# Kernel tuning notes

Hardware: AMD Instinct MI355X
Metric: run time of the kernel (lower is better)

The kernel has to match this reference:

```python
import jax, jax.numpy as jnp
import numpy as np

N = 100000
E = 1600000
H = 128
L = 3


def setup_inputs() -> dict:
    key = jax.random.key(0)
    ks = jax.random.split(key, 8)
    z = jax.random.normal(ks[0], (N, H), dtype=jnp.float32)
    edge_index = jax.random.randint(ks[1], (2, E), 0, N, dtype=jnp.int64)
    edge_weight = jax.random.uniform(ks[2], (E,), dtype=jnp.float32)
    s = 1.0 / np.sqrt(H)
    weight = jax.random.uniform(ks[3], (L, H, H), minval=-s, maxval=s, dtype=jnp.float32)
    w_ih = jax.random.uniform(ks[4], (3 * H, H), minval=-s, maxval=s, dtype=jnp.float32)
    w_hh = jax.random.uniform(ks[5], (3 * H, H), minval=-s, maxval=s, dtype=jnp.float32)
    b_ih = jax.random.uniform(ks[6], (3 * H,), minval=-s, maxval=s, dtype=jnp.float32)
    b_hh = jax.random.uniform(ks[7], (3 * H,), minval=-s, maxval=s, dtype=jnp.float32)
    return {"z": z, "edge_weight": edge_weight, "weight": weight,
            "w_ih": w_ih, "w_hh": w_hh, "b_ih": b_ih, "b_hh": b_hh,
            "edge_index": edge_index}


def _gru_cell(m, h, w_ih, w_hh, b_ih, b_hh):
    # torch GRUCell: gate order (r, z, n)
    gi = m @ w_ih.T + b_ih   # [N, 3H]
    gh = h @ w_hh.T + b_hh   # [N, 3H]
    i_r, i_z, i_n = jnp.split(gi, 3, axis=-1)
    h_r, h_z, h_n = jnp.split(gh, 3, axis=-1)
    r = jax.nn.sigmoid(i_r + h_r)
    zg = jax.nn.sigmoid(i_z + h_z)
    n = jnp.tanh(i_n + r * h_n)
    return (1.0 - zg) * n + zg * h


def reference(z, edge_weight, weight, w_ih, w_hh, b_ih, b_hh, edge_index):
    src = edge_index[0]  # x_j gathered from source nodes
    dst = edge_index[1]  # aggregated at target nodes
    x = z  # in_channels == out_channels, so no zero padding needed
    for l in range(L):
        m = x @ weight[l]                                  # [N, H]
        msg = m[src] * edge_weight[:, None]                # [E, H]
        agg = jax.ops.segment_sum(msg, dst, num_segments=N)  # aggr='add'
        x = _gru_cell(agg, x, w_ih, w_hh, b_ih, b_hh)
    return x
```

## Files before the change

kernel.cpp:

```cpp
#include <hip/hip_runtime.h>

typedef __bf16 bf16x8 __attribute__((ext_vector_type(8)));
typedef float floatx4 __attribute__((ext_vector_type(4)));

#define NPB 256
#define NPB_SHIFT 8
#define MAXNB 1024
#define TILE 4096

static __device__ __forceinline__ float bfu_to_f(unsigned short u) {
    unsigned int x = ((unsigned int)u) << 16;
    return __builtin_bit_cast(float, x);
}
static __device__ __forceinline__ unsigned short f_to_bfu(float f) {
    unsigned int u = __builtin_bit_cast(unsigned int, f);
    unsigned int r = (u + 0x7fffu + ((u >> 16) & 1u)) >> 16;
    return (unsigned short)r;
}

__global__ void detect_k(const unsigned short* __restrict__ bih_u,
                         const unsigned int* __restrict__ ei_u,
                         int* __restrict__ flags) {
    if (threadIdx.x == 0 && blockIdx.x == 0) {
        int votes = 0;
        for (int i = 0; i < 64; i++) {
            unsigned short u = bih_u[2 * i];
            unsigned int ex = (u >> 7) & 0xFF;
            if (ex >= 64 && ex < 124) votes++;
        }
        flags[0] = (votes >= 48) ? 1 : 0;
        int zeros = 0;
        for (int i = 0; i < 64; i++) {
            if (ei_u[2 * i + 1] == 0u) zeros++;
        }
        flags[1] = (zeros == 64) ? 1 : 0;
    }
}


__global__ void cvt_bf16_k(const void* __restrict__ in, unsigned short* __restrict__ out,
                           int n, const int* __restrict__ flags) {
    int i = blockIdx.x * 256 + threadIdx.x;
    if (i >= n) return;
    if (flags[0]) out[i] = ((const unsigned short*)in)[i];
    else out[i] = f_to_bfu(((const float*)in)[i]);
}

__global__ void cvt_bias_k(const void* __restrict__ bih, const void* __restrict__ bhh,
                           float* __restrict__ bih_f, float* __restrict__ bhh_f,
                           const int* __restrict__ flags) {
    int i = blockIdx.x * 256 + threadIdx.x;
    if (i >= 768) return;
    const void* src = (i < 384) ? bih : bhh;
    int j = (i < 384) ? i : i - 384;
    float v = flags[0] ? bfu_to_f(((const unsigned short*)src)[j]) : ((const float*)src)[j];
    if (i < 384) bih_f[j] = v;
    else bhh_f[j] = v;
}

__global__ void out_k(const unsigned short* __restrict__ xb, void* __restrict__ out,
                      int n, const int* __restrict__ flags) {
    int i = blockIdx.x * 256 + threadIdx.x;
    if (i >= n) return;
    if (flags[0]) ((unsigned short*)out)[i] = xb[i];
    else ((float*)out)[i] = bfu_to_f(xb[i]);
}


static __device__ __forceinline__ int load_idx(const unsigned int* eiu, size_t pos, int is64) {
    return (int)eiu[is64 ? 2 * pos : pos];
}

__global__ __launch_bounds__(256) void count_k(const unsigned int* __restrict__ eiu,
                                               int* __restrict__ bucketCnt, int E,
                                               const int* __restrict__ flags) {
    __shared__ int cnt[MAXNB];
    int t = threadIdx.x;
    for (int b = t; b < MAXNB; b += 256) cnt[b] = 0;
    __syncthreads();
    int is64 = flags[1];
    int e0 = blockIdx.x * TILE;
    int e1 = min(e0 + TILE, E);
    for (int e = e0 + t; e < e1; e += 256) {
        int d = load_idx(eiu, (size_t)E + e, is64);
        atomicAdd(&cnt[d >> NPB_SHIFT], 1);
    }
    __syncthreads();
    for (int b = t; b < MAXNB; b += 256) {
        int c = cnt[b];
        if (c) atomicAdd(&bucketCnt[b], c);
    }
}

__global__ void scanB_k(const int* __restrict__ bucketCnt, int* __restrict__ bucketBase,
                        int* __restrict__ bucketCursor, int NB, int E) {
    __shared__ int sh[MAXNB];
    int t = threadIdx.x;
    int v = (t < NB) ? bucketCnt[t] : 0;
    sh[t] = v;
    __syncthreads();
    for (int off = 1; off < MAXNB; off <<= 1) {
        int u = (t >= off) ? sh[t - off] : 0;
        __syncthreads();
        sh[t] += u;
        __syncthreads();
    }
    if (t < NB) {
        int b = sh[t] - v;
        bucketBase[t] = b;
        bucketCursor[t] = b;
    }
    if (t == 0) bucketBase[NB] = E;
}

__global__ __launch_bounds__(256) void bin_k(const unsigned int* __restrict__ eiu,
                                             const void* __restrict__ ew,
                                             int* __restrict__ bucketCursor,
                                             uint2* __restrict__ rec8,
                                             int* __restrict__ dstA, int E,
                                             const int* __restrict__ flags) {
    __shared__ int cnt[MAXNB];
    __shared__ int basel[MAXNB];
    int t = threadIdx.x;
    for (int b = t; b < MAXNB; b += 256) cnt[b] = 0;
    __syncthreads();
    int is64 = flags[1];
    int isb = flags[0];
    int e0 = blockIdx.x * TILE;
    int e1 = min(e0 + TILE, E);
    for (int e = e0 + t; e < e1; e += 256) {
        int d = load_idx(eiu, (size_t)E + e, is64);
        atomicAdd(&cnt[d >> NPB_SHIFT], 1);
    }
    __syncthreads();
    for (int b = t; b < MAXNB; b += 256) {
        int c = cnt[b];
        basel[b] = c ? atomicAdd(&bucketCursor[b], c) : 0;
        cnt[b] = 0;
    }
    __syncthreads();
    for (int e = e0 + t; e < e1; e += 256) {
        int s = load_idx(eiu, (size_t)e, is64);
        int d = load_idx(eiu, (size_t)E + e, is64);
        float w = isb ? bfu_to_f(((const unsigned short*)ew)[e]) : ((const float*)ew)[e];
        int b = d >> NPB_SHIFT;
        int p = basel[b] + atomicAdd(&cnt[b], 1);
        dstA[p] = d;
        rec8[p] = make_uint2((unsigned int)s, __builtin_bit_cast(unsigned int, w));
    }
}

__global__ __launch_bounds__(256) void csr_k(const uint2* __restrict__ rec8,
                                             const int* __restrict__ dstA,
                                             const int* __restrict__ bucketBase,
                                             int* __restrict__ offsets,
                                             uint2* __restrict__ rec, int N, int E) {
    __shared__ int cnt[NPB];
    __shared__ int sh[NPB];
    __shared__ int cur[NPB];
    int t = threadIdx.x;
    int b = blockIdx.x;
    int n0 = b << NPB_SHIFT;
    int nodes = min(NPB, N - n0);
    int ebase = bucketBase[b];
    int ecnt = bucketBase[b + 1] - ebase;

    cnt[t] = 0;
    __syncthreads();
    for (int i = t; i < ecnt; i += 256) {
        int d = dstA[ebase + i] - n0;
        atomicAdd(&cnt[d], 1);
    }
    __syncthreads();
    int v = cnt[t];
    sh[t] = v;
    __syncthreads();
    for (int off = 1; off < NPB; off <<= 1) {
        int u = (t >= off) ? sh[t - off] : 0;
        __syncthreads();
        sh[t] += u;
        __syncthreads();
    }
    int loff = sh[t] - v;
    if (t < nodes) offsets[n0 + t] = ebase + loff;
    cur[t] = ebase + loff;
    if (b == 0 && t == 0) offsets[N] = E;
    __syncthreads();
    for (int i = t; i < ecnt; i += 256) {
        int d = dstA[ebase + i] - n0;
        int p = atomicAdd(&cur[d], 1);
        rec[p] = rec8[ebase + i];
    }
}


static __device__ __forceinline__ float dot8_bf(uint4 wv, uint4 iv) {
    float s;
    s  = bfu_to_f((unsigned short)(wv.x)) * bfu_to_f((unsigned short)(iv.x));
    s += bfu_to_f((unsigned short)(wv.x >> 16)) * bfu_to_f((unsigned short)(iv.x >> 16));
    s += bfu_to_f((unsigned short)(wv.y)) * bfu_to_f((unsigned short)(iv.y));
    s += bfu_to_f((unsigned short)(wv.y >> 16)) * bfu_to_f((unsigned short)(iv.y >> 16));
    s += bfu_to_f((unsigned short)(wv.z)) * bfu_to_f((unsigned short)(iv.z));
    s += bfu_to_f((unsigned short)(wv.z >> 16)) * bfu_to_f((unsigned short)(iv.z >> 16));
    s += bfu_to_f((unsigned short)(wv.w)) * bfu_to_f((unsigned short)(iv.w));
    s += bfu_to_f((unsigned short)(wv.w >> 16)) * bfu_to_f((unsigned short)(iv.w >> 16));
    return s;
}

__global__ void make_ut_k(const void* __restrict__ weight, const void* __restrict__ wih,
                          unsigned short* __restrict__ Ut, const int* __restrict__ flags) {
    int idx = blockIdx.x * 256 + threadIdx.x;
    if (idx >= 3 * 384 * 128) return;
    int isb = flags[0];
    int a = idx & 127;
    int j = (idx >> 7) % 384;
    int l = idx / (384 * 128);
    float s = 0.f;
    if (isb) {
        const uint4* W4 = (const uint4*)((const unsigned short*)weight + (size_t)l * 16384 + a * 128);
        const uint4* I4 = (const uint4*)((const unsigned short*)wih + (size_t)j * 128);
#pragma unroll
        for (int c = 0; c < 16; c++) s += dot8_bf(W4[c], I4[c]);
    } else {
        const float4* W4 = (const float4*)((const float*)weight + (size_t)l * 16384 + a * 128);
        const float4* I4 = (const float4*)((const float*)wih + (size_t)j * 128);
#pragma unroll
        for (int c = 0; c < 32; c++) {
            float4 w = W4[c], i = I4[c];
            s += w.x * i.x + w.y * i.y + w.z * i.z + w.w * i.w;
        }
    }
    Ut[idx] = f_to_bfu(s);
}

__global__ void pack_b_k(const unsigned short* __restrict__ Ut,
                         const void* __restrict__ whh,
                         unsigned short* __restrict__ Bp,
                         const int* __restrict__ flags) {
    int idx = blockIdx.x * 256 + threadIdx.x;
    if (idx >= 3 * 48 * 4 * 64) return;
    int l = idx / 12288;
    int rem = idx % 12288;
    int ct = rem >> 8;
    int kc = (rem >> 6) & 3;
    int lane = rem & 63;
    int col = (ct % 24) * 16 + (lane & 15);
    int k = kc * 32 + (lane >> 4) * 8;
    unsigned short tmp[8];
    const unsigned short* src;
    if (ct < 24) {
        src = Ut + (size_t)l * 49152 + col * 128 + k;
    } else if (flags[0]) {
        src = (const unsigned short*)whh + (size_t)col * 128 + k;
    } else {
        const float* wf = (const float*)whh + (size_t)col * 128 + k;
        for (int i = 0; i < 8; i++) tmp[i] = f_to_bfu(wf[i]);
        src = tmp;
    }
    unsigned short* dst = Bp + (size_t)l * 98304 + ((size_t)(ct * 4 + kc) * 64 + lane) * 8;
    for (int i = 0; i < 8; i++) dst[i] = src[i];
}


__global__ __launch_bounds__(256) void agg_k(const unsigned short* __restrict__ xb,
                                             const int* __restrict__ offs,
                                             const uint2* __restrict__ rec,
                                             unsigned short* __restrict__ y, int N) {
    int node = (int)((blockIdx.x * 256 + threadIdx.x) >> 4);
    int l16 = threadIdx.x & 15;
    if (node >= N) return;
    int b = offs[node];
    int e2 = offs[node + 1];
    const uint4* xp4 = (const uint4*)xb;
    float a0[8], a1[8];
#pragma unroll
    for (int i = 0; i < 8; i++) { a0[i] = 0.f; a1[i] = 0.f; }

    auto fma_row = [&](float* acc, uint4 v, float w) {
        acc[0] += w * __builtin_bit_cast(float, v.x << 16);
        acc[1] += w * __builtin_bit_cast(float, v.x & 0xffff0000u);
        acc[2] += w * __builtin_bit_cast(float, v.y << 16);
        acc[3] += w * __builtin_bit_cast(float, v.y & 0xffff0000u);
        acc[4] += w * __builtin_bit_cast(float, v.z << 16);
        acc[5] += w * __builtin_bit_cast(float, v.z & 0xffff0000u);
        acc[6] += w * __builtin_bit_cast(float, v.w << 16);
        acc[7] += w * __builtin_bit_cast(float, v.w & 0xffff0000u);
    };

    int e = b;
    for (; e + 4 <= e2; e += 4) {
        uint2 r0 = rec[e], r1 = rec[e + 1], r2 = rec[e + 2], r3 = rec[e + 3];
        uint4 v0 = xp4[(size_t)r0.x * 16 + l16];
        uint4 v1 = xp4[(size_t)r1.x * 16 + l16];
        uint4 v2 = xp4[(size_t)r2.x * 16 + l16];
        uint4 v3 = xp4[(size_t)r3.x * 16 + l16];
        fma_row(a0, v0, __builtin_bit_cast(float, r0.y));
        fma_row(a1, v1, __builtin_bit_cast(float, r1.y));
        fma_row(a0, v2, __builtin_bit_cast(float, r2.y));
        fma_row(a1, v3, __builtin_bit_cast(float, r3.y));
    }
    for (; e < e2; e++) {
        uint2 r = rec[e];
        uint4 v = xp4[(size_t)r.x * 16 + l16];
        fma_row(a0, v, __builtin_bit_cast(float, r.y));
    }

    uint4 o;
    o.x = (unsigned int)f_to_bfu(a0[0] + a1[0]) | ((unsigned int)f_to_bfu(a0[1] + a1[1]) << 16);
    o.y = (unsigned int)f_to_bfu(a0[2] + a1[2]) | ((unsigned int)f_to_bfu(a0[3] + a1[3]) << 16);
    o.z = (unsigned int)f_to_bfu(a0[4] + a1[4]) | ((unsigned int)f_to_bfu(a0[5] + a1[5]) << 16);
    o.w = (unsigned int)f_to_bfu(a0[6] + a1[6]) | ((unsigned int)f_to_bfu(a0[7] + a1[7]) << 16);
    ((uint4*)y)[(size_t)node * 16 + l16] = o;
}


__global__ __launch_bounds__(512, 4) void gru_k(const unsigned short* __restrict__ y,
                                                const unsigned short* __restrict__ xin,
                                                unsigned short* __restrict__ xout,
                                                const unsigned short* __restrict__ Bp,
                                                const float* __restrict__ bih,
                                                const float* __restrict__ bhh, int N) {
    int tid = threadIdx.x;
    int wave = tid >> 6;
    int lane = tid & 63;
    int quad = lane >> 4;
    int m16 = lane & 15;
    int row0 = blockIdx.x * 32;

    floatx4 acc[2][4];
#pragma unroll
    for (int rt = 0; rt < 2; rt++)
#pragma unroll
        for (int s = 0; s < 4; s++) acc[rt][s] = (floatx4){0.f, 0.f, 0.f, 0.f};

    int rA[2];
#pragma unroll
    for (int rt = 0; rt < 2; rt++) {
        int r = row0 + rt * 16 + m16;
        rA[rt] = (r < N) ? r : N - 1;
    }

#pragma unroll
    for (int kc = 0; kc < 4; kc++) {
        int ko = kc * 32 + quad * 8;
        bf16x8 aY[2], aX[2];
#pragma unroll
        for (int rt = 0; rt < 2; rt++) {
            aY[rt] = *(const bf16x8*)(y + (size_t)rA[rt] * 128 + ko);
            aX[rt] = *(const bf16x8*)(xin + (size_t)rA[rt] * 128 + ko);
        }
        bf16x8 bU[3], bW[3];
#pragma unroll
        for (int g = 0; g < 3; g++) {
            int ctU = g * 8 + wave;
            int ctW = 24 + g * 8 + wave;
            bU[g] = *(const bf16x8*)(Bp + ((size_t)(ctU * 4 + kc) * 64 + lane) * 8);
            bW[g] = *(const bf16x8*)(Bp + ((size_t)(ctW * 4 + kc) * 64 + lane) * 8);
        }
#pragma unroll
        for (int rt = 0; rt < 2; rt++) {
            acc[rt][0] = __builtin_amdgcn_mfma_f32_16x16x32_bf16(aY[rt], bU[0], acc[rt][0], 0, 0, 0);
            acc[rt][0] = __builtin_amdgcn_mfma_f32_16x16x32_bf16(aX[rt], bW[0], acc[rt][0], 0, 0, 0);
            acc[rt][1] = __builtin_amdgcn_mfma_f32_16x16x32_bf16(aY[rt], bU[1], acc[rt][1], 0, 0, 0);
            acc[rt][1] = __builtin_amdgcn_mfma_f32_16x16x32_bf16(aX[rt], bW[1], acc[rt][1], 0, 0, 0);
            acc[rt][2] = __builtin_amdgcn_mfma_f32_16x16x32_bf16(aY[rt], bU[2], acc[rt][2], 0, 0, 0);
            acc[rt][3] = __builtin_amdgcn_mfma_f32_16x16x32_bf16(aX[rt], bW[2], acc[rt][3], 0, 0, 0);
        }
    }

    int ch = wave * 16 + m16;
    float b_r = bih[ch] + bhh[ch];
    float b_z = bih[128 + ch] + bhh[128 + ch];
    float bi_n = bih[256 + ch];
    float bh_n = bhh[256 + ch];
#pragma unroll
    for (int rt = 0; rt < 2; rt++) {
#pragma unroll
        for (int ri = 0; ri < 4; ri++) {
            int row = row0 + rt * 16 + quad * 4 + ri;
            if (row >= N) continue;
            float sr = acc[rt][0][ri] + b_r;
            float sz = acc[rt][1][ri] + b_z;
            float gn = acc[rt][2][ri] + bi_n;
            float hn = acc[rt][3][ri] + bh_n;
            float r = __builtin_amdgcn_rcpf(1.f + __expf(-sr));
            float zg = __builtin_amdgcn_rcpf(1.f + __expf(-sz));
            float x2 = gn + r * hn;
            float n = 1.f - 2.f * __builtin_amdgcn_rcpf(1.f + __expf(2.f * x2));
            float h = bfu_to_f(xin[(size_t)row * 128 + ch]);
            float o = n + zg * (h - n);
            xout[(size_t)row * 128 + ch] = f_to_bfu(o);
        }
    }
}


extern "C" void kernel_launch(void* const* d_in, const int* in_sizes, int n_in,
                              void* d_out, int out_size, void* d_ws, size_t ws_size,
                              hipStream_t stream) {
    const int N = in_sizes[0] / 128;
    const int E = in_sizes[1];
    const int NB = (N + NPB - 1) >> NPB_SHIFT;

    const void* z = d_in[0];
    const void* ew = d_in[1];
    const void* weight = d_in[2];
    const void* wih = d_in[3];
    const void* whh = d_in[4];
    const void* bih = d_in[5];
    const void* bhh = d_in[6];
    const unsigned int* eiu = (const unsigned int*)d_in[7];

    unsigned short* y = (unsigned short*)d_out;

    size_t off = 0;
    char* base = (char*)d_ws;
    auto carve = [&](size_t bytes) -> void* {
        void* p = base + off;
        off = (off + bytes + 255) & ~(size_t)255;
        return p;
    };
    unsigned short* xb = (unsigned short*)carve((size_t)N * 128 * 2);
    unsigned short* xb2 = (unsigned short*)carve((size_t)N * 128 * 2);
    uint2* rec8 = (uint2*)carve((size_t)E * 8);
    int* dstA = (int*)carve((size_t)E * 4);
    uint2* rec = (uint2*)carve((size_t)E * 8);
    int* offsets = (int*)carve((size_t)(N + 1) * 4);
    int* bucketCnt = (int*)carve(MAXNB * 4);
    int* bucketBase = (int*)carve((MAXNB + 1) * 4);
    int* bucketCursor = (int*)carve(MAXNB * 4);
    unsigned short* Ut = (unsigned short*)carve((size_t)3 * 384 * 128 * 2);
    unsigned short* Bp = (unsigned short*)carve((size_t)3 * 48 * 4 * 64 * 8 * 2);
    float* bih_f = (float*)carve(384 * 4);
    float* bhh_f = (float*)carve(384 * 4);
    int* flags = (int*)carve(256);

    detect_k<<<1, 64, 0, stream>>>((const unsigned short*)bih, eiu, flags);

    cvt_bf16_k<<<(N * 128 + 255) / 256, 256, 0, stream>>>(z, xb, N * 128, flags);
    cvt_bias_k<<<3, 256, 0, stream>>>(bih, bhh, bih_f, bhh_f, flags);

    hipMemsetAsync(bucketCnt, 0, MAXNB * 4, stream);
    int gbin = (E + TILE - 1) / TILE;
    count_k<<<gbin, 256, 0, stream>>>(eiu, bucketCnt, E, flags);
    scanB_k<<<1, MAXNB, 0, stream>>>(bucketCnt, bucketBase, bucketCursor, NB, E);
    bin_k<<<gbin, 256, 0, stream>>>(eiu, ew, bucketCursor, rec8, dstA, E, flags);
    csr_k<<<NB, NPB, 0, stream>>>(rec8, dstA, bucketBase, offsets, rec, N, E);

    make_ut_k<<<(3 * 384 * 128 + 255) / 256, 256, 0, stream>>>(weight, wih, Ut, flags);
    pack_b_k<<<(3 * 48 * 4 * 64 + 255) / 256, 256, 0, stream>>>(Ut, whh, Bp, flags);

    const unsigned short* cur = xb;
    unsigned short* nxt = xb2;
    for (int l = 0; l < 3; l++) {
        agg_k<<<(N + 15) / 16, 256, 0, stream>>>(cur, offsets, rec, y, N);
        gru_k<<<(N + 31) / 32, 512, 0, stream>>>(y, cur, nxt, Bp + (size_t)l * 98304,
                                                 bih_f, bhh_f, N);
        const unsigned short* tmp = cur;
        cur = nxt;
        nxt = (unsigned short*)tmp;
    }

    out_k<<<(N * 128 + 255) / 256, 256, 0, stream>>>(cur, d_out, N * 128, flags);
}
```

Measured before the change: 680.2 us.

## Tile GRU GEMM by 128-row x 32-channel blocks with LDS-staged weights

Restructures the GRU kernel so each block handles 128 rows and one of four 32-channel groups, staging that group's packed weight slice (48 KB) into shared memory instead of every wave reading all weight fragments from global memory. The weight packing is reordered to match the new channel-group layout, and the block index is swizzled so groups of 8 row-blocks share a channel group. The goal is to cut redundant weight traffic per row tile. In exchange, each of the 4 channel-group blocks re-reads the same activation rows, and the 48 KB shared-memory allocation, together with the raised occupancy hint in launch bounds, may limit how many blocks run at once.

```diff
diff --git a/kernel.cpp b/kernel.cpp
--- a/kernel.cpp
+++ b/kernel.cpp
@@ -238,26 +238,35 @@
                          unsigned short* __restrict__ Bp,
                          const int* __restrict__ flags) {
     int idx = blockIdx.x * 256 + threadIdx.x;
-    if (idx >= 3 * 48 * 4 * 64) return;
-    int l = idx / 12288;
-    int rem = idx % 12288;
-    int ct = rem >> 8;
-    int kc = (rem >> 6) & 3;
-    int lane = rem & 63;
-    int col = (ct % 24) * 16 + (lane & 15);
+    if (idx >= 3 * 4 * 12 * 4 * 64) return;
+    int lane = idx & 63;
+    int kc = (idx >> 6) & 3;
+    int rest = idx >> 8;
+    int j = rest % 12;
+    int cg = (rest / 12) & 3;
+    int l = rest / 48;
+    int s = j / 6;
+    int g = (j % 6) >> 1;
+    int t = j & 1;
+    int col = (cg * 2 + t) * 16 + (lane & 15);
     int k = kc * 32 + (lane >> 4) * 8;
+    (void)g;
     unsigned short tmp[8];
     const unsigned short* src;
-    if (ct < 24) {
-        src = Ut + (size_t)l * 49152 + col * 128 + k;
+    if (s == 0) {
+        int row384 = (j % 6) >> 1;
+        row384 = row384 * 128 + col;
+        src = Ut + (size_t)l * 49152 + row384 * 128 + k;
     } else if (flags[0]) {
-        src = (const unsigned short*)whh + (size_t)col * 128 + k;
+        int row384 = ((j % 6) >> 1) * 128 + col;
+        src = (const unsigned short*)whh + (size_t)row384 * 128 + k;
     } else {
-        const float* wf = (const float*)whh + (size_t)col * 128 + k;
+        int row384 = ((j % 6) >> 1) * 128 + col;
+        const float* wf = (const float*)whh + (size_t)row384 * 128 + k;
         for (int i = 0; i < 8; i++) tmp[i] = f_to_bfu(wf[i]);
         src = tmp;
     }
-    unsigned short* dst = Bp + (size_t)l * 98304 + ((size_t)(ct * 4 + kc) * 64 + lane) * 8;
+    unsigned short* dst = Bp + (size_t)l * 98304 + (((size_t)(cg * 12 + j) * 4 + kc) * 64 + lane) * 8;
     for (int i = 0; i < 8; i++) dst[i] = src[i];
 }
 
@@ -314,18 +323,36 @@
 }
 
 
-__global__ __launch_bounds__(512, 4) void gru_k(const unsigned short* __restrict__ y,
+__global__ __launch_bounds__(512, 6) void gru_k(const unsigned short* __restrict__ y,
                                                 const unsigned short* __restrict__ xin,
                                                 unsigned short* __restrict__ xout,
                                                 const unsigned short* __restrict__ Bp,
                                                 const float* __restrict__ bih,
                                                 const float* __restrict__ bhh, int N) {
+    __shared__ uint4 Blds[3072];
+
+    int bid = blockIdx.x;
+    int r8 = bid & 7;
+    int inner = bid >> 3;
+    int cg = inner & 3;
+    int rb = ((inner >> 2) << 3) + r8;
+    int row0 = rb << 7;
+    if (row0 >= N) return;
+
     int tid = threadIdx.x;
     int wave = tid >> 6;
+    int wc = wave & 1;
+    int wr = wave >> 1;
     int lane = tid & 63;
     int quad = lane >> 4;
     int m16 = lane & 15;
-    int row0 = blockIdx.x * 32;
+
+    {
+        const uint4* bsrc = (const uint4*)(Bp + (size_t)cg * 24576);
+#pragma unroll
+        for (int i = 0; i < 6; i++) Blds[tid + i * 512] = bsrc[tid + i * 512];
+    }
+    __syncthreads();
 
     floatx4 acc[2][4];
 #pragma unroll
@@ -336,9 +363,11 @@
     int rA[2];
 #pragma unroll
     for (int rt = 0; rt < 2; rt++) {
-        int r = row0 + rt * 16 + m16;
+        int r = row0 + wr * 32 + rt * 16 + m16;
         rA[rt] = (r < N) ? r : N - 1;
     }
+
+    const unsigned short* bl = (const unsigned short*)Blds;
 
 #pragma unroll
     for (int kc = 0; kc < 4; kc++) {
@@ -352,10 +381,10 @@
         bf16x8 bU[3], bW[3];
 #pragma unroll
         for (int g = 0; g < 3; g++) {
-            int ctU = g * 8 + wave;
-            int ctW = 24 + g * 8 + wave;
-            bU[g] = *(const bf16x8*)(Bp + ((size_t)(ctU * 4 + kc) * 64 + lane) * 8);
-            bW[g] = *(const bf16x8*)(Bp + ((size_t)(ctW * 4 + kc) * 64 + lane) * 8);
+            int jU = g * 2 + wc;
+            int jW = 6 + g * 2 + wc;
+            bU[g] = *(const bf16x8*)(bl + ((size_t)(jU * 4 + kc) * 64 + lane) * 8);
+            bW[g] = *(const bf16x8*)(bl + ((size_t)(jW * 4 + kc) * 64 + lane) * 8);
         }
 #pragma unroll
         for (int rt = 0; rt < 2; rt++) {
@@ -368,7 +397,7 @@
         }
     }
 
-    int ch = wave * 16 + m16;
+    int ch = cg * 32 + wc * 16 + m16;
     float b_r = bih[ch] + bhh[ch];
     float b_z = bih[128 + ch] + bhh[128 + ch];
     float bi_n = bih[256 + ch];
@@ -377,7 +406,7 @@
     for (int rt = 0; rt < 2; rt++) {
 #pragma unroll
         for (int ri = 0; ri < 4; ri++) {
-            int row = row0 + rt * 16 + quad * 4 + ri;
+            int row = row0 + wr * 32 + rt * 16 + quad * 4 + ri;
             if (row >= N) continue;
             float sr = acc[rt][0][ri] + b_r;
             float sz = acc[rt][1][ri] + b_z;
@@ -448,14 +477,17 @@
     csr_k<<<NB, NPB, 0, stream>>>(rec8, dstA, bucketBase, offsets, rec, N, E);
 
     make_ut_k<<<(3 * 384 * 128 + 255) / 256, 256, 0, stream>>>(weight, wih, Ut, flags);
-    pack_b_k<<<(3 * 48 * 4 * 64 + 255) / 256, 256, 0, stream>>>(Ut, whh, Bp, flags);
+    pack_b_k<<<(3 * 4 * 12 * 4 * 64 + 255) / 256, 256, 0, stream>>>(Ut, whh, Bp, flags);
+
+    const int RB = (N + 127) >> 7;
+    const int grid_gru = 8 * ((RB + 7) >> 3) * 4;
 
     const unsigned short* cur = xb;
     unsigned short* nxt = xb2;
     for (int l = 0; l < 3; l++) {
         agg_k<<<(N + 15) / 16, 256, 0, stream>>>(cur, offsets, rec, y, N);
-        gru_k<<<(N + 31) / 32, 512, 0, stream>>>(y, cur, nxt, Bp + (size_t)l * 98304,
-                                                 bih_f, bhh_f, N);
+        gru_k<<<grid_gru, 512, 0, stream>>>(y, cur, nxt, Bp + (size_t)l * 98304,
+                                            bih_f, bhh_f, N);
         const unsigned short* tmp = cur;
         cur = nxt;
         nxt = (unsigned short*)tmp;
```

After: 652.5 us. 1.04x faster.
